# Performance work log

Hardware: AMD Instinct MI355X
Metric: run time of the kernel (lower is better)

## Reference

```python
import jax, jax.numpy as jnp
import numpy as np

B, N, F_IN, F_E, H, L = 8, 128, 64, 16, 256, 8
EPS = 1e-5


def _linear_params(key, fan_in, fan_out):
    k1, k2 = jax.random.split(key)
    bound = 1.0 / np.sqrt(fan_in)
    W = jax.random.uniform(k1, (fan_in, fan_out), minval=-bound, maxval=bound, dtype=jnp.float32)
    b = jax.random.uniform(k2, (fan_out,), minval=-bound, maxval=bound, dtype=jnp.float32)
    return W, b


def setup_inputs() -> dict:
    key = jax.random.key(0)
    ks = jax.random.split(key, 16)
    x = jax.random.normal(ks[0], (B, N, F_IN), dtype=jnp.float32)
    adj = jax.random.randint(ks[1], (B, N, N), 0, 2, dtype=jnp.int32)
    edge_attr = jax.random.normal(ks[2], (B, N, N, F_E), dtype=jnp.float32)
    mask = jnp.ones((B, N), dtype=jnp.int32)

    node_W, node_b = _linear_params(ks[3], F_IN, H)
    edge_W, edge_b = _linear_params(ks[4], F_E, H)

    lks = jax.random.split(ks[5], L)
    W1s, b1s, W2s, b2s = [], [], [], []
    for i in range(L):
        a, b_ = jax.random.split(lks[i])
        W1, b1 = _linear_params(a, H, H)
        W2, b2 = _linear_params(b_, H, H)
        W1s.append(W1); b1s.append(b1); W2s.append(W2); b2s.append(b2)
    ln_g = jnp.ones((L, H), dtype=jnp.float32)
    ln_b = jnp.zeros((L, H), dtype=jnp.float32)
    W1 = jnp.stack(W1s); b1 = jnp.stack(b1s)
    W2 = jnp.stack(W2s); b2 = jnp.stack(b2s)

    ro_pW, ro_pb = _linear_params(ks[6], H, H)
    ro_aW, ro_ab = _linear_params(ks[7], H, 1)
    ph_W, ph_b = _linear_params(ks[8], H, 1)

    return dict(x=x, adj=adj, edge_attr=edge_attr, mask=mask,
                node_W=node_W, node_b=node_b, edge_W=edge_W, edge_b=edge_b,
                ln_g=ln_g, ln_b=ln_b, W1=W1, b1=b1, W2=W2, b2=b2,
                ro_pW=ro_pW, ro_pb=ro_pb, ro_aW=ro_aW, ro_ab=ro_ab,
                ph_W=ph_W, ph_b=ph_b)


def _layernorm(x, g, b):
    mu = jnp.mean(x, axis=-1, keepdims=True)
    var = jnp.var(x, axis=-1, keepdims=True)
    return (x - mu) * jax.lax.rsqrt(var + EPS) * g + b


def _gine_forward(x, adjf, edge_attr, maskf,
                  node_W, node_b, edge_W, edge_b,
                  ln_g, ln_b, W1, b1, W2, b2,
                  ro_pW, ro_pb, ro_aW, ro_ab, ph_W, ph_b):
    h = x @ node_W + node_b                      # (B,N,H)
    edge_emb = edge_attr @ edge_W + edge_b       # (B,N,N,H)
    m = maskf[..., None]                         # (B,N,1)

    def layer(h, p):
        g, bln, w1, bb1, w2, bb2 = p
        h = h * m
        h_norm = _layernorm(h, g, bln)
        # message: h_j + e_ij, j indexes axis 2 -> broadcast over axis 1
        m_in = h_norm[:, None, :, :] + edge_emb          # (B,N,N,H)
        mm = jax.nn.relu(jax.nn.relu(m_in @ w1 + bb1) @ w2 + bb2)
        mm = mm * adjf[..., None]
        msg = mm.sum(axis=2)                             # (B,N,H)
        out = (h + msg) * m
        return out, None

    h, _ = jax.lax.scan(layer, h, (ln_g, ln_b, W1, b1, W2, b2))

    # attention readout
    hp = jnp.tanh(h @ ro_pW + ro_pb)
    scores = (hp @ ro_aW).squeeze(-1) + ro_ab            # (B,N)
    scores = jnp.where(maskf > 0, scores, -jnp.inf)
    alpha = jax.nn.softmax(scores, axis=1)
    cnt = jnp.clip(maskf.sum(axis=1, keepdims=True), 1.0, None)
    fallback = jnp.where(maskf > 0, 1.0 / cnt, 0.0)
    alpha = jnp.where(jnp.isnan(alpha), fallback, alpha)
    gvec = (h * alpha[..., None]).sum(axis=1)            # (B,H)
    out = (gvec @ ph_W + ph_b).squeeze(-1)               # (B,)
    return out


def reference(x, adj, edge_attr, mask,
              node_W, node_b, edge_W, edge_b,
              ln_g, ln_b, W1, b1, W2, b2,
              ro_pW, ro_pb, ro_aW, ro_ab, ph_W, ph_b):
    adjf = adj.astype(jnp.float32)
    maskf = mask.astype(jnp.float32)
    return _gine_forward(x, adjf, edge_attr, maskf,
                         node_W, node_b, edge_W, edge_b,
                         ln_g, ln_b, W1, b1, W2, b2,
                         ro_pW, ro_pb, ro_aW, ro_ab, ph_W, ph_b)
```

## Files before the change

### kernel.cpp

```cpp
#include <hip/hip_runtime.h>

typedef float  f32x4  __attribute__((ext_vector_type(4)));
typedef short  bf16x8 __attribute__((ext_vector_type(8)));
typedef unsigned short u16;
typedef unsigned int   u32;

static __device__ __forceinline__ u16 f2bf(float f) {
    u32 u = __float_as_uint(f);
    u += 0x7FFFu + ((u >> 16) & 1u);
    return (u16)(u >> 16);
}



__global__ void k_h0ln(const float* __restrict__ x, const float* __restrict__ nW,
                       const float* __restrict__ nb, const int* __restrict__ mask,
                       const float* __restrict__ lng, const float* __restrict__ lnb,
                       float* __restrict__ h, u16* __restrict__ hnbf) {
    __shared__ float xr[64];
    __shared__ float rs[4], rs2[4];
    int row = blockIdx.x, c = threadIdx.x;
    if (c < 64) xr[c] = x[row * 64 + c];
    __syncthreads();
    float acc = nb[c];
#pragma unroll
    for (int k = 0; k < 64; ++k) acc += xr[k] * nW[k * 256 + c];
    float mv = (float)mask[row];
    float v = acc * mv;
    h[row * 256 + c] = v;
    float s = v, s2 = v * v;
    int w = c >> 6, lane = c & 63;
#pragma unroll
    for (int off = 32; off; off >>= 1) {
        s  += __shfl_xor(s,  off);
        s2 += __shfl_xor(s2, off);
    }
    if (lane == 0) { rs[w] = s; rs2[w] = s2; }
    __syncthreads();
    float S  = rs[0] + rs[1] + rs[2] + rs[3];
    float S2 = rs2[0] + rs2[1] + rs2[2] + rs2[3];
    float mu  = S * (1.f / 256.f);
    float var = S2 * (1.f / 256.f) - mu * mu;
    float rstd = rsqrtf(var + 1e-5f);
    hnbf[row * 256 + c] = f2bf((v - mu) * rstd * lng[c] + lnb[c]);
}

__global__ void k_edgefrag(const float* __restrict__ ea, u16* __restrict__ ef) {
    int gid = blockIdx.x * 256 + threadIdx.x;
    int lane = gid & 63, nt = (gid >> 6) & 7, i = (gid >> 9) & 127, b = gid >> 16;
    int j = nt * 16 + (lane & 15), k0 = (lane >> 4) * 8;
    uint4 out = {0u, 0u, 0u, 0u};
    if (k0 < 16) {
        const float* p = ea + (((size_t)(b * 128 + i) * 128 + j) * 16 + k0);
        u16 us[8];
#pragma unroll
        for (int t = 0; t < 8; ++t) us[t] = f2bf(p[t]);
        out.x = (u32)us[0] | ((u32)us[1] << 16);
        out.y = (u32)us[2] | ((u32)us[3] << 16);
        out.z = (u32)us[4] | ((u32)us[5] << 16);
        out.w = (u32)us[6] | ((u32)us[7] << 16);
    }
    ((uint4*)ef)[gid] = out;
}

__global__ void k_wt(const float* __restrict__ W1, const float* __restrict__ W2,
                     u16* __restrict__ w1t, u16* __restrict__ w2t) {
    int gid = blockIdx.x * 256 + threadIdx.x;
    int lane = gid & 63, mt = (gid >> 6) & 15, kt = (gid >> 10) & 7, l = gid >> 13;
    int hh = mt * 16 + (lane & 15), k = kt * 32 + (lane >> 4) * 8;
    u16 a[8], b[8];
#pragma unroll
    for (int t = 0; t < 8; ++t) {
        size_t idx = (size_t)l * 65536 + (size_t)(k + t) * 256 + hh;
        a[t] = f2bf(W1[idx]);
        b[t] = f2bf(W2[idx]);
    }
    uint4 oa, ob;
    oa.x = (u32)a[0] | ((u32)a[1] << 16); oa.y = (u32)a[2] | ((u32)a[3] << 16);
    oa.z = (u32)a[4] | ((u32)a[5] << 16); oa.w = (u32)a[6] | ((u32)a[7] << 16);
    ob.x = (u32)b[0] | ((u32)b[1] << 16); ob.y = (u32)b[2] | ((u32)b[3] << 16);
    ob.z = (u32)b[4] | ((u32)b[5] << 16); ob.w = (u32)b[6] | ((u32)b[7] << 16);
    ((uint4*)w1t)[gid] = oa;
    ((uint4*)w2t)[gid] = ob;
}

__global__ void k_wf1b(const float* __restrict__ eW, const float* __restrict__ eb,
                       const float* __restrict__ W1, const float* __restrict__ b1,
                       u16* __restrict__ wf, float* __restrict__ bias1) {
    __shared__ float eWsT[256 * 16];
    __shared__ float ebS[256];
    int l = blockIdx.x, tid = threadIdx.x;
#pragma unroll
    for (int k = 0; k < 16; ++k) eWsT[tid * 16 + k] = eW[k * 256 + tid];
    ebS[tid] = eb[tid];
    __syncthreads();
    float acc[16];
#pragma unroll
    for (int k = 0; k < 16; ++k) acc[k] = 0.f;
    float bacc = b1[l * 256 + tid];
    const float* w1c = W1 + (size_t)l * 65536 + tid;
    for (int c = 0; c < 256; ++c) {
        float wv = w1c[(size_t)c * 256];
        const f32x4* e = (const f32x4*)&eWsT[c * 16];
#pragma unroll
        for (int q = 0; q < 4; ++q) {
            f32x4 ev = e[q];
#pragma unroll
            for (int t = 0; t < 4; ++t) acc[q * 4 + t] += ev[t] * wv;
        }
        bacc += ebS[c] * wv;
    }
    bias1[l * 256 + tid] = bacc;
    int mt = tid >> 4, lo = tid & 15;
#pragma unroll
    for (int c4 = 0; c4 < 4; ++c4) {
        u16 us[8];
#pragma unroll
        for (int t = 0; t < 8; ++t) {
            int k = c4 * 8 + t;
            us[t] = (k < 16) ? f2bf(acc[k]) : (u16)0;
        }
        uint4 o;
        o.x = (u32)us[0] | ((u32)us[1] << 16);
        o.y = (u32)us[2] | ((u32)us[3] << 16);
        o.z = (u32)us[4] | ((u32)us[5] << 16);
        o.w = (u32)us[6] | ((u32)us[7] << 16);
        ((uint4*)wf)[(size_t)(l * 16 + mt) * 64 + c4 * 16 + lo] = o;
    }
}


__global__ __launch_bounds__(256) void k_hn1(const u16* __restrict__ w1t,
        const u16* __restrict__ hnbf, const float* __restrict__ bias1,
        float* __restrict__ hn1p, int l) {
    int orig = blockIdx.x;
    int bid = (orig & 7) * 16 + (orig >> 3);
    int b = bid >> 4, mt = bid & 15;
    int tid = threadIdx.x, w = tid >> 6, lane = tid & 63;
    f32x4 bv = *(const f32x4*)(bias1 + l * 256 + mt * 16 + (lane >> 4) * 4);
    f32x4 acc0 = bv, acc1 = bv;
    int j0 = (w * 2) * 16 + (lane & 15), j1 = j0 + 16;
#pragma unroll
    for (int kt = 0; kt < 8; ++kt) {
        bf16x8 a = *(const bf16x8*)(w1t + ((size_t)((l * 8 + kt) * 16 + mt) * 64 + lane) * 8);
        bf16x8 bt0 = *(const bf16x8*)(hnbf + ((size_t)(b * 128 + j0) * 256 + kt * 32 + (lane >> 4) * 8));
        bf16x8 bt1 = *(const bf16x8*)(hnbf + ((size_t)(b * 128 + j1) * 256 + kt * 32 + (lane >> 4) * 8));
        acc0 = __builtin_amdgcn_mfma_f32_16x16x32_bf16(a, bt0, acc0, 0, 0, 0);
        acc1 = __builtin_amdgcn_mfma_f32_16x16x32_bf16(a, bt1, acc1, 0, 0, 0);
    }
    float* outb = hn1p + (size_t)b * 32768;
    *(f32x4*)(outb + ((size_t)(mt * 8 + w * 2) * 64 + lane) * 4)     = acc0;
    *(f32x4*)(outb + ((size_t)(mt * 8 + w * 2 + 1) * 64 + lane) * 4) = acc1;
}

__global__ __launch_bounds__(512, 4) void k_msg(
        const u16* __restrict__ wf1t, const u16* __restrict__ ef,
        const u16* __restrict__ w2t,  const float* __restrict__ hn1p,
        const float* __restrict__ b2, const int* __restrict__ adj,
        const int* __restrict__ mask, float* __restrict__ h,
        const float* __restrict__ lngN, const float* __restrict__ lnbN,
        u16* __restrict__ hnbf, int l, int doLN) {

    __shared__ __align__(16) u16  t1S[8 * 8 * 64 * 8];
    __shared__ __align__(16) float b2S[256];
    __shared__ __align__(16) float msgS[256];
    __shared__ int listS[128];
    __shared__ int flagS[128];
    __shared__ int cntS;
    __shared__ float rs[8], rs2[8];

    int orig = blockIdx.x;
    int bid = (orig & 7) * 128 + (orig >> 3);
    int b = bid >> 7, i = bid & 127;
    int tid = threadIdx.x, w = tid >> 6, lane = tid & 63;
    int row = b * 128 + i;

    if (tid < 128) { flagS[tid] = adj[(size_t)row * 128 + tid]; listS[tid] = 0; }
    if (tid < 256) b2S[tid] = b2[l * 256 + tid];
    __syncthreads();

    if (w == 0) {
        int f0 = flagS[lane], f1 = flagS[64 + lane];
        unsigned long long m0 = __ballot(f0 != 0);
        unsigned long long m1 = __ballot(f1 != 0);
        unsigned long long lt = (1ull << lane) - 1ull;
        int c0 = __popcll(m0);
        if (f0) listS[__popcll(m0 & lt)] = lane;
        if (f1) listS[c0 + __popcll(m1 & lt)] = 64 + lane;
        if (lane == 0) cntS = c0 + __popcll(m1);
    }
    __syncthreads();
    int cnt = cntS;
    int NT = (cnt + 15) >> 4;

    const u16*  efb = ef + (size_t)row * 4096;
    const float* hpb = hn1p + (size_t)b * 32768;
    int mt0 = w * 2, mt1 = w * 2 + 1;
    bf16x8 aG0 = *(const bf16x8*)(wf1t + ((size_t)(l * 16 + mt0) * 64 + lane) * 8);
    bf16x8 aG1 = *(const bf16x8*)(wf1t + ((size_t)(l * 16 + mt1) * 64 + lane) * 8);
    for (int n = 0; n < NT; ++n) {
        int j = listS[n * 16 + (lane & 15)];
        int jo = (j >> 4) * 64 + (lane & 48) + (j & 15);
        bf16x8 be = *(const bf16x8*)(efb + (size_t)jo * 8);
        {
            f32x4 ci = *(const f32x4*)(hpb + ((size_t)(mt0 * 8) * 64 + jo) * 4);
            f32x4 acc = __builtin_amdgcn_mfma_f32_16x16x32_bf16(aG0, be, ci, 0, 0, 0);
            u32 lo = (u32)f2bf(fmaxf(acc[0], 0.f)) | ((u32)f2bf(fmaxf(acc[1], 0.f)) << 16);
            u32 hi = (u32)f2bf(fmaxf(acc[2], 0.f)) | ((u32)f2bf(fmaxf(acc[3], 0.f)) << 16);
            int g = ((mt0 & 1) << 1) | (lane >> 5), half = (lane >> 4) & 1;
            uint2 pk; pk.x = lo; pk.y = hi;
            *(uint2*)(t1S + ((size_t)((w * 8 + n) * 64) + g * 16 + (lane & 15)) * 8 + half * 4) = pk;
        }
        {
            f32x4 ci = *(const f32x4*)(hpb + ((size_t)(mt1 * 8) * 64 + jo) * 4);
            f32x4 acc = __builtin_amdgcn_mfma_f32_16x16x32_bf16(aG1, be, ci, 0, 0, 0);
            u32 lo = (u32)f2bf(fmaxf(acc[0], 0.f)) | ((u32)f2bf(fmaxf(acc[1], 0.f)) << 16);
            u32 hi = (u32)f2bf(fmaxf(acc[2], 0.f)) | ((u32)f2bf(fmaxf(acc[3], 0.f)) << 16);
            int g = ((mt1 & 1) << 1) | (lane >> 5), half = (lane >> 4) & 1;
            uint2 pk; pk.x = lo; pk.y = hi;
            *(uint2*)(t1S + ((size_t)((w * 8 + n) * 64) + g * 16 + (lane & 15)) * 8 + half * 4) = pk;
        }
    }
    __syncthreads();

    bf16x8 a2[8][2];
#pragma unroll
    for (int kt = 0; kt < 8; ++kt) {
        a2[kt][0] = *(const bf16x8*)(w2t + ((size_t)((l * 8 + kt) * 16 + mt0) * 64 + lane) * 8);
        a2[kt][1] = *(const bf16x8*)(w2t + ((size_t)((l * 8 + kt) * 16 + mt1) * 64 + lane) * 8);
    }
    int hb0 = mt0 * 16 + (lane >> 4) * 4;
    int hb1 = mt1 * 16 + (lane >> 4) * 4;
    f32x4 bv0 = *(const f32x4*)(&b2S[hb0]);
    f32x4 bv1 = *(const f32x4*)(&b2S[hb1]);
    f32x4 ms0 = (f32x4){0.f, 0.f, 0.f, 0.f};
    f32x4 ms1 = (f32x4){0.f, 0.f, 0.f, 0.f};
    for (int n = 0; n < NT; ++n) {
        f32x4 acc0 = (f32x4){0.f, 0.f, 0.f, 0.f};
        f32x4 acc1 = (f32x4){0.f, 0.f, 0.f, 0.f};
#pragma unroll
        for (int kt = 0; kt < 8; ++kt) {
            bf16x8 bt = *(const bf16x8*)(t1S + ((size_t)(kt * 8 + n) * 64 + lane) * 8);
            acc0 = __builtin_amdgcn_mfma_f32_16x16x32_bf16(a2[kt][0], bt, acc0, 0, 0, 0);
            acc1 = __builtin_amdgcn_mfma_f32_16x16x32_bf16(a2[kt][1], bt, acc1, 0, 0, 0);
        }
        float aw = (n * 16 + (lane & 15)) < cnt ? 1.f : 0.f;
#pragma unroll
        for (int r = 0; r < 4; ++r) {
            ms0[r] += fmaxf(acc0[r] + bv0[r], 0.f) * aw;
            ms1[r] += fmaxf(acc1[r] + bv1[r], 0.f) * aw;
        }
    }
#pragma unroll
    for (int r = 0; r < 4; ++r) {
        ms0[r] += __shfl_xor(ms0[r], 1); ms1[r] += __shfl_xor(ms1[r], 1);
        ms0[r] += __shfl_xor(ms0[r], 2); ms1[r] += __shfl_xor(ms1[r], 2);
        ms0[r] += __shfl_xor(ms0[r], 4); ms1[r] += __shfl_xor(ms1[r], 4);
        ms0[r] += __shfl_xor(ms0[r], 8); ms1[r] += __shfl_xor(ms1[r], 8);
    }
    if ((lane & 15) == 0) {
        *(f32x4*)(&msgS[hb0]) = ms0;
        *(f32x4*)(&msgS[hb1]) = ms1;
    }
    __syncthreads();

    float v = 0.f;
    if (tid < 256) {
        float mv = (float)mask[row];
        v = (h[(size_t)row * 256 + tid] + msgS[tid]) * mv;
        h[(size_t)row * 256 + tid] = v;
    }
    float s = v, s2 = v * v;
#pragma unroll
    for (int off = 32; off; off >>= 1) {
        s  += __shfl_xor(s,  off);
        s2 += __shfl_xor(s2, off);
    }
    if (lane == 0) { rs[w] = s; rs2[w] = s2; }
    __syncthreads();
    if (doLN && tid < 256) {
        float S = 0.f, S2 = 0.f;
#pragma unroll
        for (int t = 0; t < 8; ++t) { S += rs[t]; S2 += rs2[t]; }
        float mu  = S * (1.f / 256.f);
        float var = S2 * (1.f / 256.f) - mu * mu;
        float rstd = rsqrtf(var + 1e-5f);
        hnbf[(size_t)row * 256 + tid] = f2bf((v - mu) * rstd * lngN[tid] + lnbN[tid]);
    }
}


__global__ void k_ro1(const float* __restrict__ h, const float* __restrict__ pW,
                      const float* __restrict__ pb, const float* __restrict__ aW,
                      const float* __restrict__ ab, float* __restrict__ scores) {
    __shared__ float hr[8][256];
    __shared__ float red[4][8];
    int blk = blockIdx.x, b = blk >> 4, g = blk & 15;
    int tid = threadIdx.x;
    size_t base = (size_t)(b * 128 + g * 8) * 256;
#pragma unroll
    for (int t = 0; t < 8; ++t) hr[t][tid] = h[base + t * 256 + tid];
    __syncthreads();
    float facc[8];
    float pbv = pb[tid];
#pragma unroll
    for (int j = 0; j < 8; ++j) facc[j] = pbv;
    for (int k = 0; k < 256; ++k) {
        float wv = pW[(size_t)k * 256 + tid];
#pragma unroll
        for (int j = 0; j < 8; ++j) facc[j] += hr[j][k] * wv;
    }
    float awc = aW[tid];
    int w = tid >> 6, lane = tid & 63;
#pragma unroll
    for (int j = 0; j < 8; ++j) {
        float v = tanhf(facc[j]) * awc;
#pragma unroll
        for (int off = 32; off; off >>= 1) v += __shfl_xor(v, off);
        if (lane == 0) red[w][j] = v;
    }
    __syncthreads();
    if (tid < 8)
        scores[b * 128 + g * 8 + tid] = red[0][tid] + red[1][tid] + red[2][tid] + red[3][tid] + ab[0];
}

__global__ void k_ro2(const float* __restrict__ h, const float* __restrict__ scores,
                      const int* __restrict__ mask, const float* __restrict__ phW,
                      const float* __restrict__ phb, float* __restrict__ out) {
    __shared__ float aS[128];
    __shared__ float rm[4], rc[4], red[4];
    int b = blockIdx.x, tid = threadIdx.x, w = tid >> 6, lane = tid & 63;
    float mv = 0.f, sv = -__builtin_inff();
    if (tid < 128) {
        mv = (float)mask[b * 128 + tid];
        if (mv > 0.f) sv = scores[b * 128 + tid];
    }
    float mx = sv, cs = mv;
#pragma unroll
    for (int off = 32; off; off >>= 1) {
        mx = fmaxf(mx, __shfl_xor(mx, off));
        cs += __shfl_xor(cs, off);
    }
    if (lane == 0) { rm[w] = mx; rc[w] = cs; }
    __syncthreads();
    mx = fmaxf(fmaxf(rm[0], rm[1]), fmaxf(rm[2], rm[3]));
    float cnt = rc[0] + rc[1] + rc[2] + rc[3];
    float e = (tid < 128 && mv > 0.f) ? expf(sv - mx) : 0.f;
    float se = e;
#pragma unroll
    for (int off = 32; off; off >>= 1) se += __shfl_xor(se, off);
    if (lane == 0) red[w] = se;
    __syncthreads();
    float S = red[0] + red[1] + red[2] + red[3];
    if (tid < 128) {
        float a;
        if (S > 0.f) a = e / S;
        else         a = (mv > 0.f) ? 1.f / fmaxf(cnt, 1.f) : 0.f;
        aS[tid] = a;
    }
    __syncthreads();
    float g = 0.f;
    const float* hb = h + (size_t)b * 128 * 256;
    for (int n = 0; n < 128; ++n) g += aS[n] * hb[(size_t)n * 256 + tid];
    float p = g * phW[tid];
#pragma unroll
    for (int off = 32; off; off >>= 1) p += __shfl_xor(p, off);
    __syncthreads();
    if (lane == 0) red[w] = p;
    __syncthreads();
    if (tid == 0) out[b] = red[0] + red[1] + red[2] + red[3] + phb[0];
}

extern "C" void kernel_launch(void* const* d_in, const int* in_sizes, int n_in,
                              void* d_out, int out_size, void* d_ws, size_t ws_size,
                              hipStream_t stream) {
    const float* x    = (const float*)d_in[0];
    const int*   adj  = (const int*)  d_in[1];
    const float* ea   = (const float*)d_in[2];
    const int*   mask = (const int*)  d_in[3];
    const float* nW   = (const float*)d_in[4];
    const float* nb   = (const float*)d_in[5];
    const float* eW   = (const float*)d_in[6];
    const float* eb   = (const float*)d_in[7];
    const float* lng  = (const float*)d_in[8];
    const float* lnb  = (const float*)d_in[9];
    const float* W1   = (const float*)d_in[10];
    const float* b1   = (const float*)d_in[11];
    const float* W2   = (const float*)d_in[12];
    const float* b2   = (const float*)d_in[13];
    const float* ropW = (const float*)d_in[14];
    const float* ropb = (const float*)d_in[15];
    const float* roaW = (const float*)d_in[16];
    const float* roab = (const float*)d_in[17];
    const float* phW  = (const float*)d_in[18];
    const float* phb  = (const float*)d_in[19];
    float* out = (float*)d_out;

    char* p = (char*)d_ws;
    auto alloc = [&](size_t bytes) { char* r = p; p += (bytes + 255) & ~(size_t)255; return r; };
    float* h     = (float*)alloc((size_t)8 * 128 * 256 * 4);
    u16*   hnbf  = (u16*)  alloc((size_t)8 * 128 * 256 * 2);
    float* hn1p  = (float*)alloc((size_t)8 * 32768 * 4);
    u16*   ef    = (u16*)  alloc((size_t)8 * 128 * 4096 * 2);
    u16*   wf1t  = (u16*)  alloc((size_t)8 * 16 * 64 * 8 * 2);
    u16*   w1t   = (u16*)  alloc((size_t)8 * 8 * 16 * 64 * 8 * 2);
    u16*   w2t   = (u16*)  alloc((size_t)8 * 8 * 16 * 64 * 8 * 2);
    float* bias1 = (float*)alloc((size_t)8 * 256 * 4);
    float* scores= (float*)alloc((size_t)1024 * 4);

    k_h0ln    <<<1024, 256, 0, stream>>>(x, nW, nb, mask, lng, lnb, h, hnbf);
    k_edgefrag<<<2048, 256, 0, stream>>>(ea, ef);
    k_wt      <<<256,  256, 0, stream>>>(W1, W2, w1t, w2t);
    k_wf1b    <<<8,    256, 0, stream>>>(eW, eb, W1, b1, wf1t, bias1);

    for (int l = 0; l < 8; ++l) {
        k_hn1<<<128,  256, 0, stream>>>(w1t, hnbf, bias1, hn1p, l);
        int doLN = (l < 7) ? 1 : 0;
        int ln_next = (l < 7) ? (l + 1) : l;
        k_msg<<<1024, 512, 0, stream>>>(wf1t, ef, w2t, hn1p, b2, adj, mask, h,
                                        lng + ln_next * 256, lnb + ln_next * 256,
                                        hnbf, l, doLN);
    }

    k_ro1<<<128, 256, 0, stream>>>(h, ropW, ropb, roaW, roab, scores);
    k_ro2<<<8,   256, 0, stream>>>(h, scores, mask, phW, phb, out);
}
```

Baseline: 355.8 us.

## Retile message kernel warps over node groups and move readout projection to MFMA

The message kernel now gives each wave four output tiles and half of the neighbor tiles, where before each wave had two tiles and all neighbors. W2 fragments are loaded from global inside the loop instead of being held in registers, and the two partial message sums are combined through shared memory. The adjacency flags are read straight into the ballot, which removes one shared buffer and one barrier. The readout projection becomes a bf16 MFMA kernel over the final hidden state, which the last layer now writes in bf16 without layernorm, using a new pre-transposed weight kernel. This trades the fp32 scalar loop for lower precision and adds reloads of W2 per neighbor tile.

```diff
diff --git a/kernel.cpp b/kernel.cpp
--- a/kernel.cpp
+++ b/kernel.cpp
@@ -82,6 +82,19 @@
     ob.z = (u32)b[4] | ((u32)b[5] << 16); ob.w = (u32)b[6] | ((u32)b[7] << 16);
     ((uint4*)w1t)[gid] = oa;
     ((uint4*)w2t)[gid] = ob;
+}
+
+__global__ void k_pwt(const float* __restrict__ pW, u16* __restrict__ pwt) {
+    int gid = blockIdx.x * 256 + threadIdx.x;
+    int lane = gid & 63, mt = (gid >> 6) & 15, kt = gid >> 10;
+    int hh = mt * 16 + (lane & 15), k = kt * 32 + (lane >> 4) * 8;
+    u16 a[8];
+#pragma unroll
+    for (int t = 0; t < 8; ++t) a[t] = f2bf(pW[(size_t)(k + t) * 256 + hh]);
+    uint4 o;
+    o.x = (u32)a[0] | ((u32)a[1] << 16); o.y = (u32)a[2] | ((u32)a[3] << 16);
+    o.z = (u32)a[4] | ((u32)a[5] << 16); o.w = (u32)a[6] | ((u32)a[7] << 16);
+    ((uint4*)pwt)[gid] = o;
 }
 
 __global__ void k_wf1b(const float* __restrict__ eW, const float* __restrict__ eb,
@@ -163,9 +176,8 @@
 
     __shared__ __align__(16) u16  t1S[8 * 8 * 64 * 8];
     __shared__ __align__(16) float b2S[256];
-    __shared__ __align__(16) float msgS[256];
+    __shared__ __align__(16) float msgS[2][256];
     __shared__ int listS[128];
-    __shared__ int flagS[128];
     __shared__ int cntS;
     __shared__ float rs[8], rs2[8];
 
@@ -173,14 +185,14 @@
     int bid = (orig & 7) * 128 + (orig >> 3);
     int b = bid >> 7, i = bid & 127;
     int tid = threadIdx.x, w = tid >> 6, lane = tid & 63;
+    int mq = w & 3, ng = w >> 2;
     int row = b * 128 + i;
 
-    if (tid < 128) { flagS[tid] = adj[(size_t)row * 128 + tid]; listS[tid] = 0; }
     if (tid < 256) b2S[tid] = b2[l * 256 + tid];
-    __syncthreads();
-
     if (w == 0) {
-        int f0 = flagS[lane], f1 = flagS[64 + lane];
+        listS[lane] = 0; listS[64 + lane] = 0;
+        int f0 = adj[(size_t)row * 128 + lane];
+        int f1 = adj[(size_t)row * 128 + 64 + lane];
         unsigned long long m0 = __ballot(f0 != 0);
         unsigned long long m1 = __ballot(f1 != 0);
         unsigned long long lt = (1ull << lane) - 1ull;
@@ -195,79 +207,74 @@
 
     const u16*  efb = ef + (size_t)row * 4096;
     const float* hpb = hn1p + (size_t)b * 32768;
-    int mt0 = w * 2, mt1 = w * 2 + 1;
-    bf16x8 aG0 = *(const bf16x8*)(wf1t + ((size_t)(l * 16 + mt0) * 64 + lane) * 8);
-    bf16x8 aG1 = *(const bf16x8*)(wf1t + ((size_t)(l * 16 + mt1) * 64 + lane) * 8);
-    for (int n = 0; n < NT; ++n) {
+    bf16x8 aG[4];
+#pragma unroll
+    for (int m = 0; m < 4; ++m)
+        aG[m] = *(const bf16x8*)(wf1t + ((size_t)(l * 16 + mq * 4 + m) * 64 + lane) * 8);
+    for (int n = ng; n < NT; n += 2) {
         int j = listS[n * 16 + (lane & 15)];
         int jo = (j >> 4) * 64 + (lane & 48) + (j & 15);
         bf16x8 be = *(const bf16x8*)(efb + (size_t)jo * 8);
-        {
-            f32x4 ci = *(const f32x4*)(hpb + ((size_t)(mt0 * 8) * 64 + jo) * 4);
-            f32x4 acc = __builtin_amdgcn_mfma_f32_16x16x32_bf16(aG0, be, ci, 0, 0, 0);
+#pragma unroll
+        for (int m = 0; m < 4; ++m) {
+            int mt = mq * 4 + m;
+            f32x4 ci = *(const f32x4*)(hpb + ((size_t)(mt * 8) * 64 + jo) * 4);
+            f32x4 acc = __builtin_amdgcn_mfma_f32_16x16x32_bf16(aG[m], be, ci, 0, 0, 0);
             u32 lo = (u32)f2bf(fmaxf(acc[0], 0.f)) | ((u32)f2bf(fmaxf(acc[1], 0.f)) << 16);
             u32 hi = (u32)f2bf(fmaxf(acc[2], 0.f)) | ((u32)f2bf(fmaxf(acc[3], 0.f)) << 16);
-            int g = ((mt0 & 1) << 1) | (lane >> 5), half = (lane >> 4) & 1;
+            int g = ((mt & 1) << 1) | (lane >> 5), half = (lane >> 4) & 1;
             uint2 pk; pk.x = lo; pk.y = hi;
-            *(uint2*)(t1S + ((size_t)((w * 8 + n) * 64) + g * 16 + (lane & 15)) * 8 + half * 4) = pk;
-        }
-        {
-            f32x4 ci = *(const f32x4*)(hpb + ((size_t)(mt1 * 8) * 64 + jo) * 4);
-            f32x4 acc = __builtin_amdgcn_mfma_f32_16x16x32_bf16(aG1, be, ci, 0, 0, 0);
-            u32 lo = (u32)f2bf(fmaxf(acc[0], 0.f)) | ((u32)f2bf(fmaxf(acc[1], 0.f)) << 16);
-            u32 hi = (u32)f2bf(fmaxf(acc[2], 0.f)) | ((u32)f2bf(fmaxf(acc[3], 0.f)) << 16);
-            int g = ((mt1 & 1) << 1) | (lane >> 5), half = (lane >> 4) & 1;
-            uint2 pk; pk.x = lo; pk.y = hi;
-            *(uint2*)(t1S + ((size_t)((w * 8 + n) * 64) + g * 16 + (lane & 15)) * 8 + half * 4) = pk;
-        }
-    }
-    __syncthreads();
-
-    bf16x8 a2[8][2];
-#pragma unroll
-    for (int kt = 0; kt < 8; ++kt) {
-        a2[kt][0] = *(const bf16x8*)(w2t + ((size_t)((l * 8 + kt) * 16 + mt0) * 64 + lane) * 8);
-        a2[kt][1] = *(const bf16x8*)(w2t + ((size_t)((l * 8 + kt) * 16 + mt1) * 64 + lane) * 8);
-    }
-    int hb0 = mt0 * 16 + (lane >> 4) * 4;
-    int hb1 = mt1 * 16 + (lane >> 4) * 4;
-    f32x4 bv0 = *(const f32x4*)(&b2S[hb0]);
-    f32x4 bv1 = *(const f32x4*)(&b2S[hb1]);
-    f32x4 ms0 = (f32x4){0.f, 0.f, 0.f, 0.f};
-    f32x4 ms1 = (f32x4){0.f, 0.f, 0.f, 0.f};
-    for (int n = 0; n < NT; ++n) {
-        f32x4 acc0 = (f32x4){0.f, 0.f, 0.f, 0.f};
-        f32x4 acc1 = (f32x4){0.f, 0.f, 0.f, 0.f};
+            *(uint2*)(t1S + ((size_t)(((mt >> 1) * 8 + n) * 64) + g * 16 + (lane & 15)) * 8 + half * 4) = pk;
+        }
+    }
+    __syncthreads();
+
+    f32x4 bv[4], ms[4];
+#pragma unroll
+    for (int m = 0; m < 4; ++m) {
+        bv[m] = *(const f32x4*)(&b2S[(mq * 4 + m) * 16 + (lane >> 4) * 4]);
+        ms[m] = (f32x4){0.f, 0.f, 0.f, 0.f};
+    }
+    for (int n = ng; n < NT; n += 2) {
+        f32x4 acc[4];
+#pragma unroll
+        for (int m = 0; m < 4; ++m) acc[m] = (f32x4){0.f, 0.f, 0.f, 0.f};
 #pragma unroll
         for (int kt = 0; kt < 8; ++kt) {
             bf16x8 bt = *(const bf16x8*)(t1S + ((size_t)(kt * 8 + n) * 64 + lane) * 8);
-            acc0 = __builtin_amdgcn_mfma_f32_16x16x32_bf16(a2[kt][0], bt, acc0, 0, 0, 0);
-            acc1 = __builtin_amdgcn_mfma_f32_16x16x32_bf16(a2[kt][1], bt, acc1, 0, 0, 0);
+#pragma unroll
+            for (int m = 0; m < 4; ++m) {
+                bf16x8 a2 = *(const bf16x8*)(w2t + ((size_t)((l * 8 + kt) * 16 + mq * 4 + m) * 64 + lane) * 8);
+                acc[m] = __builtin_amdgcn_mfma_f32_16x16x32_bf16(a2, bt, acc[m], 0, 0, 0);
+            }
         }
         float aw = (n * 16 + (lane & 15)) < cnt ? 1.f : 0.f;
 #pragma unroll
+        for (int m = 0; m < 4; ++m)
+#pragma unroll
+            for (int r = 0; r < 4; ++r)
+                ms[m][r] += fmaxf(acc[m][r] + bv[m][r], 0.f) * aw;
+    }
+#pragma unroll
+    for (int m = 0; m < 4; ++m)
+#pragma unroll
         for (int r = 0; r < 4; ++r) {
-            ms0[r] += fmaxf(acc0[r] + bv0[r], 0.f) * aw;
-            ms1[r] += fmaxf(acc1[r] + bv1[r], 0.f) * aw;
-        }
-    }
-#pragma unroll
-    for (int r = 0; r < 4; ++r) {
-        ms0[r] += __shfl_xor(ms0[r], 1); ms1[r] += __shfl_xor(ms1[r], 1);
-        ms0[r] += __shfl_xor(ms0[r], 2); ms1[r] += __shfl_xor(ms1[r], 2);
-        ms0[r] += __shfl_xor(ms0[r], 4); ms1[r] += __shfl_xor(ms1[r], 4);
-        ms0[r] += __shfl_xor(ms0[r], 8); ms1[r] += __shfl_xor(ms1[r], 8);
-    }
+            ms[m][r] += __shfl_xor(ms[m][r], 1);
+            ms[m][r] += __shfl_xor(ms[m][r], 2);
+            ms[m][r] += __shfl_xor(ms[m][r], 4);
+            ms[m][r] += __shfl_xor(ms[m][r], 8);
+        }
     if ((lane & 15) == 0) {
-        *(f32x4*)(&msgS[hb0]) = ms0;
-        *(f32x4*)(&msgS[hb1]) = ms1;
+#pragma unroll
+        for (int m = 0; m < 4; ++m)
+            *(f32x4*)(&msgS[ng][(mq * 4 + m) * 16 + (lane >> 4) * 4]) = ms[m];
     }
     __syncthreads();
 
     float v = 0.f;
     if (tid < 256) {
         float mv = (float)mask[row];
-        v = (h[(size_t)row * 256 + tid] + msgS[tid]) * mv;
+        v = (h[(size_t)row * 256 + tid] + msgS[0][tid] + msgS[1][tid]) * mv;
         h[(size_t)row * 256 + tid] = v;
     }
     float s = v, s2 = v * v;
@@ -278,50 +285,51 @@
     }
     if (lane == 0) { rs[w] = s; rs2[w] = s2; }
     __syncthreads();
-    if (doLN && tid < 256) {
-        float S = 0.f, S2 = 0.f;
-#pragma unroll
-        for (int t = 0; t < 8; ++t) { S += rs[t]; S2 += rs2[t]; }
-        float mu  = S * (1.f / 256.f);
-        float var = S2 * (1.f / 256.f) - mu * mu;
-        float rstd = rsqrtf(var + 1e-5f);
-        hnbf[(size_t)row * 256 + tid] = f2bf((v - mu) * rstd * lngN[tid] + lnbN[tid]);
-    }
-}
-
-
-__global__ void k_ro1(const float* __restrict__ h, const float* __restrict__ pW,
-                      const float* __restrict__ pb, const float* __restrict__ aW,
-                      const float* __restrict__ ab, float* __restrict__ scores) {
-    __shared__ float hr[8][256];
-    __shared__ float red[4][8];
-    int blk = blockIdx.x, b = blk >> 4, g = blk & 15;
-    int tid = threadIdx.x;
-    size_t base = (size_t)(b * 128 + g * 8) * 256;
-#pragma unroll
-    for (int t = 0; t < 8; ++t) hr[t][tid] = h[base + t * 256 + tid];
-    __syncthreads();
-    float facc[8];
-    float pbv = pb[tid];
-#pragma unroll
-    for (int j = 0; j < 8; ++j) facc[j] = pbv;
-    for (int k = 0; k < 256; ++k) {
-        float wv = pW[(size_t)k * 256 + tid];
-#pragma unroll
-        for (int j = 0; j < 8; ++j) facc[j] += hr[j][k] * wv;
-    }
-    float awc = aW[tid];
-    int w = tid >> 6, lane = tid & 63;
-#pragma unroll
-    for (int j = 0; j < 8; ++j) {
-        float v = tanhf(facc[j]) * awc;
-#pragma unroll
-        for (int off = 32; off; off >>= 1) v += __shfl_xor(v, off);
-        if (lane == 0) red[w][j] = v;
-    }
-    __syncthreads();
-    if (tid < 8)
-        scores[b * 128 + g * 8 + tid] = red[0][tid] + red[1][tid] + red[2][tid] + red[3][tid] + ab[0];
+    if (tid < 256) {
+        float o;
+        if (doLN) {
+            float S = 0.f, S2 = 0.f;
+#pragma unroll
+            for (int t = 0; t < 8; ++t) { S += rs[t]; S2 += rs2[t]; }
+            float mu  = S * (1.f / 256.f);
+            float var = S2 * (1.f / 256.f) - mu * mu;
+            float rstd = rsqrtf(var + 1e-5f);
+            o = (v - mu) * rstd * lngN[tid] + lnbN[tid];
+        } else o = v;
+        hnbf[(size_t)row * 256 + tid] = f2bf(o);
+    }
+}
+
+
+__global__ __launch_bounds__(512) void k_ro1(const u16* __restrict__ hbf,
+        const u16* __restrict__ pwt, const float* __restrict__ pb,
+        const float* __restrict__ aW, const float* __restrict__ ab,
+        float* __restrict__ scores) {
+    int b = blockIdx.x;
+    int tid = threadIdx.x, w = tid >> 6, lane = tid & 63;
+    f32x4 acc[16];
+#pragma unroll
+    for (int mt = 0; mt < 16; ++mt)
+        acc[mt] = *(const f32x4*)(pb + mt * 16 + (lane >> 4) * 4);
+#pragma unroll
+    for (int kt = 0; kt < 8; ++kt) {
+        bf16x8 bt = *(const bf16x8*)(hbf + ((size_t)(b * 128 + w * 16 + (lane & 15)) * 256 + kt * 32 + (lane >> 4) * 8));
+#pragma unroll
+        for (int mt = 0; mt < 16; ++mt) {
+            bf16x8 a = *(const bf16x8*)(pwt + ((size_t)(kt * 16 + mt) * 64 + lane) * 8);
+            acc[mt] = __builtin_amdgcn_mfma_f32_16x16x32_bf16(a, bt, acc[mt], 0, 0, 0);
+        }
+    }
+    float sc = 0.f;
+#pragma unroll
+    for (int mt = 0; mt < 16; ++mt) {
+#pragma unroll
+        for (int r = 0; r < 4; ++r)
+            sc += tanhf(acc[mt][r]) * aW[mt * 16 + (lane >> 4) * 4 + r];
+    }
+    sc += __shfl_xor(sc, 16);
+    sc += __shfl_xor(sc, 32);
+    if (lane < 16) scores[b * 128 + w * 16 + lane] = sc + ab[0];
 }
 
 __global__ void k_ro2(const float* __restrict__ h, const float* __restrict__ scores,
@@ -405,6 +413,7 @@
     u16*   wf1t  = (u16*)  alloc((size_t)8 * 16 * 64 * 8 * 2);
     u16*   w1t   = (u16*)  alloc((size_t)8 * 8 * 16 * 64 * 8 * 2);
     u16*   w2t   = (u16*)  alloc((size_t)8 * 8 * 16 * 64 * 8 * 2);
+    u16*   pwt   = (u16*)  alloc((size_t)8 * 16 * 64 * 8 * 2);
     float* bias1 = (float*)alloc((size_t)8 * 256 * 4);
     float* scores= (float*)alloc((size_t)1024 * 4);
 
@@ -412,6 +421,7 @@
     k_edgefrag<<<2048, 256, 0, stream>>>(ea, ef);
     k_wt      <<<256,  256, 0, stream>>>(W1, W2, w1t, w2t);
     k_wf1b    <<<8,    256, 0, stream>>>(eW, eb, W1, b1, wf1t, bias1);
+    k_pwt     <<<32,   256, 0, stream>>>(ropW, pwt);
 
     for (int l = 0; l < 8; ++l) {
         k_hn1<<<128,  256, 0, stream>>>(w1t, hnbf, bias1, hn1p, l);
@@ -422,6 +432,6 @@
                                         hnbf, l, doLN);
     }
 
-    k_ro1<<<128, 256, 0, stream>>>(h, ropW, ropb, roaW, roab, scores);
+    k_ro1<<<8,   512, 0, stream>>>(hnbf, pwt, ropb, roaW, roab, scores);
     k_ro2<<<8,   256, 0, stream>>>(h, scores, mask, phW, phb, out);
 }
```

Result: slower. 844.0 us (+137.2%).
